# Kernel optimization log

Measured on AMD Instinct MI355X. Metric: run time of the kernel, lower is better.

The kernel has to match this reference:

```python
import jax, jax.numpy as jnp
import numpy as np

N = 8192      # total nodes (32 graphs x 256 nodes)
B = 32        # graphs in batch
E = 65536     # edges per graph (avg degree 16)
DK = 512      # d_k = d_v
H = 32        # mlp / conv channel width
VB = 2048     # body visual dim
VF = 512      # face visual dim
EPS = 1e-5


def setup_inputs() -> dict:
    key = jax.random.key(0)
    ks = jax.random.split(key, 26)
    def n(k, sh, s=1.0):
        return jax.random.normal(k, sh, dtype=jnp.float32) * s
    s2, s512, s32 = 1.0 / np.sqrt(2.0), 1.0 / np.sqrt(512.0), 1.0 / np.sqrt(32.0)
    inp = {}
    inp["x"] = n(ks[0], (N, 2))
    inp["visual_body"] = n(ks[1], (N, VB))
    inp["visual_face"] = n(ks[2], (N, VF))
    # attention projections (no bias)
    inp["Wq"] = n(ks[3], (2, DK), s2)
    inp["Wk"] = n(ks[4], (2, DK), s2)
    inp["Wv"] = n(ks[5], (2, DK), s2)
    # input_mlp: LayerNorm(512) -> PReLU -> Linear(512,32)
    inp["ln_g"] = jnp.ones((DK,), jnp.float32)
    inp["ln_b"] = jnp.zeros((DK,), jnp.float32)
    inp["prelu_a"] = jnp.float32(0.25)
    inp["mlp_W"] = n(ks[6], (DK, H), s512)
    inp["mlp_b"] = jnp.zeros((H,), jnp.float32)
    # node projection Linear(32,1)
    inp["np_W"] = n(ks[7], (H, 1), s32)
    inp["np_b"] = jnp.zeros((1,), jnp.float32)
    # CMCosConv linear weights (32->32) for body / face
    inp["body_W"] = n(ks[8], (H, H), s32)
    inp["body_b"] = jnp.zeros((H,), jnp.float32)
    inp["face_W"] = n(ks[9], (H, H), s32)
    inp["face_b"] = jnp.zeros((H,), jnp.float32)
    # gcn projections Linear(32,1)
    inp["pb_W"] = n(ks[10], (H, 1), s32)
    inp["pb_b"] = jnp.zeros((1,), jnp.float32)
    inp["pf_W"] = n(ks[11], (H, 1), s32)
    inp["pf_b"] = jnp.zeros((1,), jnp.float32)
    # int-valued graph structure
    inp["edge_index_body"] = jax.random.randint(ks[12], (2, E), 0, N)
    inp["edge_index_face"] = jax.random.randint(ks[13], (2, E), 0, N)
    inp["batch_vec"] = jnp.arange(N, dtype=jnp.int64) // (N // B)  # 32 graphs, 256 nodes each
    return inp


def cmcos_conv(x, edge_index, visual, W, b):
    # per-edge cosine(visual_src, visual_dst) * Linear(x_src), scatter-sum to dst
    src, dst = edge_index[0], edge_index[1]
    h = x @ W + b                                          # [N, H]
    vn = visual * jax.lax.rsqrt(jnp.sum(visual * visual, -1, keepdims=True) + 1e-8)
    w = jnp.sum(vn[src] * vn[dst], axis=-1)                # [E] cosine edge weights
    msg = w[:, None] * h[src]                              # [E, H]
    return jax.ops.segment_sum(msg, dst, num_segments=x.shape[0])


def reference(x, visual_body, visual_face, Wq, Wk, Wv, ln_g, ln_b, prelu_a,
              mlp_W, mlp_b, np_W, np_b, body_W, body_b, face_W, face_b,
              pb_W, pb_b, pf_W, pf_b, edge_index_body, edge_index_face, batch_vec):
    sz_b = int(batch_vec[-1]) + 1
    q = (x @ Wq).reshape(sz_b, -1, DK)
    k = (x @ Wk).reshape(sz_b, -1, DK)
    v = (x @ Wv).reshape(sz_b, -1, DK)
    attn = jax.nn.softmax(jnp.einsum('bqd,bkd->bqk', q, k) / np.sqrt(DK), axis=-1)
    out = jnp.einsum('bqk,bkd->bqd', attn, v).reshape(-1, DK)   # [N, 512]
    # input_mlp: LayerNorm -> PReLU -> Linear (dropout is identity in eval)
    mu = jnp.mean(out, -1, keepdims=True)
    var = jnp.mean((out - mu) ** 2, -1, keepdims=True)
    h = (out - mu) * jax.lax.rsqrt(var + EPS) * ln_g + ln_b
    h = jnp.where(h >= 0, h, prelu_a * h)
    h = h @ mlp_W + mlp_b                                       # [N, 32]
    nodes_scores = (h @ np_W + np_b)[:, 0]
    hb = cmcos_conv(h, edge_index_body, visual_body, body_W, body_b)
    hf = cmcos_conv(h, edge_index_face, visual_face, face_W, face_b)
    gcn_scores_body = (hb @ pb_W + pb_b)[:, 0]
    gcn_scores_face = (hf @ pf_W + pf_b)[:, 0]
    return nodes_scores + gcn_scores_body + gcn_scores_face
```

## Files before the change

### kernel.cpp

```cpp
#include <hip/hip_runtime.h>

#define NN 8192
#define NB 32
#define NG 256
#define NE 65536
#define DK 512
#define HC 32
#define DB 2048
#define DF 512

#define BODY_DW (NN*DB/4)
#define FACE_DW (NN*DF/4)
#define B_BODY (BODY_DW/2048)
#define B_FACE (FACE_DW/2048)

typedef float v2f __attribute__((ext_vector_type(2)));

#if __has_builtin(__builtin_amdgcn_cvt_pk_f32_fp8) && __has_builtin(__builtin_amdgcn_cvt_pk_fp8_f32)
#define HW_FP8 1
#else
#define HW_FP8 0
#endif

__device__ __forceinline__ float fp8_dec(unsigned u) {
    unsigned e = (u >> 3) & 15u, m = u & 7u, s = u & 0x80u;
    float v = e ? __uint_as_float(((e + 120u) << 23) | (m << 20))
                : (float)m * 0.001953125f;
    return s ? -v : v;
}
__device__ __forceinline__ unsigned fp8_enc(float x) {
    unsigned sb = (__float_as_uint(x) >> 24) & 0x80u;
    float a = fabsf(x);
    if (a >= 448.f) return sb | 0x7Eu;
    if (a < 0.015625f) {
        int c = (int)rintf(a * 512.f);
        if (c > 7) return sb | 0x08u;
        return sb | (unsigned)c;
    }
    int ex; (void)frexpf(a, &ex);
    float p = ldexpf(a, 1 - ex);
    int m = (int)rintf((p - 1.f) * 8.f);
    int e = ex - 1 + 7;
    if (m == 8) { m = 0; e++; }
    if (e >= 16) return sb | 0x7Eu;
    return sb | (unsigned)(e << 3) | (unsigned)m;
}
__device__ __forceinline__ unsigned pack4_fp8(float x, float y, float z, float w) {
#if HW_FP8
    int u = __builtin_amdgcn_cvt_pk_fp8_f32(x, y, 0, false);
    u = __builtin_amdgcn_cvt_pk_fp8_f32(z, w, u, true);
    return (unsigned)u;
#else
    return fp8_enc(x) | (fp8_enc(y) << 8) | (fp8_enc(z) << 16) | (fp8_enc(w) << 24);
#endif
}
__device__ __forceinline__ float fp8dot4(unsigned a, unsigned b) {
#if HW_FP8
    v2f al = __builtin_amdgcn_cvt_pk_f32_fp8((int)a, false);
    v2f ah = __builtin_amdgcn_cvt_pk_f32_fp8((int)a, true);
    v2f bl = __builtin_amdgcn_cvt_pk_f32_fp8((int)b, false);
    v2f bh = __builtin_amdgcn_cvt_pk_f32_fp8((int)b, true);
    return al.x*bl.x + al.y*bl.y + ah.x*bh.x + ah.y*bh.y;
#else
    float s = 0.f;
    #pragma unroll
    for (int j = 0; j < 4; j++)
        s += fp8_dec((a >> (8*j)) & 255u) * fp8_dec((b >> (8*j)) & 255u);
    return s;
#endif
}
__device__ __forceinline__ float fp8dot16(int4 a, int4 b) {
    return fp8dot4((unsigned)a.x, (unsigned)b.x) + fp8dot4((unsigned)a.y, (unsigned)b.y)
         + fp8dot4((unsigned)a.z, (unsigned)b.z) + fp8dot4((unsigned)a.w, (unsigned)b.w);
}
__device__ __forceinline__ float d4(float4 v) {
    return v.x*v.x + v.y*v.y + v.z*v.z + v.w*v.w;
}

struct Params {
    const float *vb, *vf, *x, *Wq, *Wk, *Wv, *ln_g, *ln_b, *prelu_a;
    const float *mlp_W, *mlp_b, *np_W, *np_b, *body_W, *body_b, *face_W, *face_b;
    const float *pb_W, *pb_b, *pf_W, *pf_b;
    const int *eib, *eif;
    unsigned *vnb, *vnf;
    float *invb, *invf;
    float *a_ws, *sb, *sf, *fused;
    float *out;
};

__global__ __launch_bounds__(256, 4) void k1_kernel(Params p) {
    __shared__ float2 xs[NG];
    __shared__ float pm[4][4];
    __shared__ float sm4[4];
    __shared__ float rss[16];
    const int bid = blockIdx.x, tid = threadIdx.x;
    const int lane = tid & 63, wave = tid >> 6;

    if (bid < B_BODY + B_FACE) {
        const bool body = bid < B_BODY;
        const float4* __restrict__ src = body ? (const float4*)p.vb : (const float4*)p.vf;
        unsigned* __restrict__ dst = body ? p.vnb : p.vnf;
        const int base = (body ? bid : bid - B_BODY) * 2048 + tid;
        if (tid < 16) rss[tid] = 0.f;
        __syncthreads();
        float4 v0 = src[base];
        float4 v1 = src[base + 256];
        float4 v2 = src[base + 512];
        float4 v3 = src[base + 768];
        float4 v4 = src[base + 1024];
        float4 v5 = src[base + 1280];
        float4 v6 = src[base + 1536];
        float4 v7 = src[base + 1792];
        dst[base]        = pack4_fp8(v0.x, v0.y, v0.z, v0.w);
        dst[base + 256]  = pack4_fp8(v1.x, v1.y, v1.z, v1.w);
        dst[base + 512]  = pack4_fp8(v2.x, v2.y, v2.z, v2.w);
        dst[base + 768]  = pack4_fp8(v3.x, v3.y, v3.z, v3.w);
        dst[base + 1024] = pack4_fp8(v4.x, v4.y, v4.z, v4.w);
        dst[base + 1280] = pack4_fp8(v5.x, v5.y, v5.z, v5.w);
        dst[base + 1536] = pack4_fp8(v6.x, v6.y, v6.z, v6.w);
        dst[base + 1792] = pack4_fp8(v7.x, v7.y, v7.z, v7.w);
        if (body) {
            float sq[4];
            sq[0] = d4(v0) + d4(v1);
            sq[1] = d4(v2) + d4(v3);
            sq[2] = d4(v4) + d4(v5);
            sq[3] = d4(v6) + d4(v7);
            #pragma unroll
            for (int r = 0; r < 4; r++) {
                float ss = sq[r];
                #pragma unroll
                for (int off = 32; off > 0; off >>= 1) ss += __shfl_xor(ss, off);
                if (lane == 0) atomicAdd(&rss[r], ss);
            }
            __syncthreads();
            if (tid < 4) p.invb[bid*4 + tid] = rsqrtf(rss[tid] + 1e-8f);
        } else {
            float sq[8] = {d4(v0), d4(v1), d4(v2), d4(v3), d4(v4), d4(v5), d4(v6), d4(v7)};
            #pragma unroll
            for (int j = 0; j < 8; j++) {
                float ss = sq[j];
                #pragma unroll
                for (int off = 32; off > 0; off >>= 1) ss += __shfl_xor(ss, off);
                if (lane == 0) atomicAdd(&rss[(wave >> 1) + 2*j], ss);
            }
            __syncthreads();
            if (tid < 16) p.invf[(bid - B_BODY)*16 + tid] = rsqrtf(rss[tid] + 1e-8f);
        }
        return;
    }
    if (bid < B_BODY + B_FACE + NB) {
        const int gg = bid - (B_BODY + B_FACE);
        xs[tid] = ((const float2*)p.x)[gg*NG + tid];
        const int d = tid * 2;
        float q0a = p.Wq[d],    q0b = p.Wq[d+1];
        float q1a = p.Wq[DK+d], q1b = p.Wq[DK+d+1];
        float k0a = p.Wk[d],    k0b = p.Wk[d+1];
        float k1a = p.Wk[DK+d], k1b = p.Wk[DK+d+1];
        float m00 = q0a*k0a + q0b*k0b;
        float m01 = q0a*k1a + q0b*k1b;
        float m10 = q1a*k0a + q1b*k0b;
        float m11 = q1a*k1a + q1b*k1b;
        #pragma unroll
        for (int off = 32; off > 0; off >>= 1) {
            m00 += __shfl_down(m00,off); m01 += __shfl_down(m01,off);
            m10 += __shfl_down(m10,off); m11 += __shfl_down(m11,off);
        }
        if (lane == 0) { pm[wave][0]=m00; pm[wave][1]=m01; pm[wave][2]=m10; pm[wave][3]=m11; }
        __syncthreads();
        if (tid < 4) sm4[tid] = pm[0][tid] + pm[1][tid] + pm[2][tid] + pm[3][tid];
        __syncthreads();
        const float scale = 0.04419417382415922f;
        const float2 xi = xs[tid];
        const float u0 = (xi.x*sm4[0] + xi.y*sm4[2]) * scale;
        const float u1 = (xi.x*sm4[1] + xi.y*sm4[3]) * scale;
        float m = -1e30f;
        for (int j = 0; j < NG; j++) m = fmaxf(m, u0*xs[j].x + u1*xs[j].y);
        float S = 0.f, a0 = 0.f, a1 = 0.f;
        for (int j = 0; j < NG; j++) {
            float2 xj = xs[j];
            float pr = __expf(u0*xj.x + u1*xj.y - m);
            S += pr; a0 += pr*xj.x; a1 += pr*xj.y;
        }
        const float invS = 1.f / S;
        ((float2*)p.a_ws)[gg*NG + tid] = make_float2(a0*invS, a1*invS);
        return;
    }
    if (tid < HC) {
        float s = 0.f;
        #pragma unroll 8
        for (int c = 0; c < HC; c++) s += p.body_W[tid*HC + c] * p.pb_W[c];
        p.fused[tid] = s;
    } else if (tid < 2*HC) {
        const int cp = tid - HC;
        float s = 0.f;
        #pragma unroll 8
        for (int c = 0; c < HC; c++) s += p.face_W[cp*HC + c] * p.pf_W[c];
        p.fused[HC + cp] = s;
    } else if (tid == 2*HC) {
        float s = 0.f;
        for (int c = 0; c < HC; c++) s += p.body_b[c] * p.pb_W[c];
        p.fused[64] = s;
    } else if (tid == 2*HC + 1) {
        float s = 0.f;
        for (int c = 0; c < HC; c++) s += p.face_b[c] * p.pf_W[c];
        p.fused[65] = s;
    }
}

__global__ __launch_bounds__(256) void k2_kernel(Params p) {
    __shared__ float t[4][DK];
    const int tid = threadIdx.x;
    const int wave = tid >> 6, lane = tid & 63;
    const int node = blockIdx.x * 4 + wave;

    const float a0 = p.a_ws[node*2], a1 = p.a_ws[node*2+1];
    const float4* wv0 = (const float4*)p.Wv;
    const float4* wv1 = (const float4*)(p.Wv + DK);
    const float4* g4 = (const float4*)p.ln_g;
    const float4* b4 = (const float4*)p.ln_b;
    float4 W0[2], W1[2], Gg[2], Bb[2];
    #pragma unroll
    for (int k = 0; k < 2; k++) {
        int c4 = lane*2 + k;
        W0[k] = wv0[c4]; W1[k] = wv1[c4]; Gg[k] = g4[c4]; Bb[k] = b4[c4];
    }
    float s0=0.f, s1=0.f, q00=0.f, q01=0.f, q11=0.f;
    #pragma unroll
    for (int k = 0; k < 2; k++) {
        const float* u = (const float*)&W0[k];
        const float* v = (const float*)&W1[k];
        #pragma unroll
        for (int j = 0; j < 4; j++) {
            s0 += u[j]; s1 += v[j];
            q00 += u[j]*u[j]; q01 += u[j]*v[j]; q11 += v[j]*v[j];
        }
    }
    #pragma unroll
    for (int off = 1; off < 64; off <<= 1) {
        s0 += __shfl_xor(s0,off); s1 += __shfl_xor(s1,off);
        q00 += __shfl_xor(q00,off); q01 += __shfl_xor(q01,off); q11 += __shfl_xor(q11,off);
    }
    const float mean = (a0*s0 + a1*s1) * (1.f/DK);
    const float msq  = (a0*a0*q00 + 2.f*a0*a1*q01 + a1*a1*q11) * (1.f/DK);
    const float inv  = rsqrtf(msq - mean*mean + 1e-5f);
    const float alpha = p.prelu_a[0];
    #pragma unroll
    for (int k = 0; k < 2; k++) {
        int c4 = lane*2 + k;
        const float* u = (const float*)&W0[k];
        const float* v = (const float*)&W1[k];
        const float* gf = (const float*)&Gg[k];
        const float* bf = (const float*)&Bb[k];
        #pragma unroll
        for (int j = 0; j < 4; j++) {
            float od = a0*u[j] + a1*v[j];
            float nd = (od - mean) * inv * gf[j] + bf[j];
            t[wave][c4*4 + j] = (nd >= 0.f) ? nd : alpha*nd;
        }
    }
    __syncthreads();
    const int c = lane & 31, half = lane >> 5;
    const float* tp = t[wave] + half*256;
    const float* mw = p.mlp_W + half*256*HC + c;
    float p0=0.f, p1=0.f, p2=0.f, p3=0.f;
    #pragma unroll 4
    for (int d = 0; d < 256; d += 4) {
        p0 += tp[d]   * mw[d*HC];
        p1 += tp[d+1] * mw[(d+1)*HC];
        p2 += tp[d+2] * mw[(d+2)*HC];
        p3 += tp[d+3] * mw[(d+3)*HC];
    }
    float partl = (p0+p1) + (p2+p3);
    partl += __shfl_down(partl, 32);
    float v0 = 0.f, v1 = 0.f, v2 = 0.f;
    if (lane < 32) {
        float hc = partl + p.mlp_b[c];
        v0 = hc * p.np_W[c];
        v1 = hc * p.fused[c];
        v2 = hc * p.fused[HC + c];
    }
    #pragma unroll
    for (int off = 16; off > 0; off >>= 1) {
        v0 += __shfl_down(v0, off);
        v1 += __shfl_down(v1, off);
        v2 += __shfl_down(v2, off);
    }
    if (lane == 0) {
        p.out[node] = v0 + p.np_b[0] + p.pb_b[0] + p.pf_b[0];
        p.sb[node] = v1 + p.fused[64];
        p.sf[node] = v2 + p.fused[65];
    }
}

__global__ __launch_bounds__(256) void scat_kernel(Params p) {
    const int wave = threadIdx.x >> 6, lane = threadIdx.x & 63;
    if (blockIdx.x < NE/8) {
        const int e = blockIdx.x * 8 + wave * 2;
        const int sA = p.eib[e],     dA = p.eib[NE + e];
        const int sB = p.eib[e + 1], dB = p.eib[NE + e + 1];
        const int4* ap0 = (const int4*)(p.vnb + (size_t)sA * (DB/4));
        const int4* bp0 = (const int4*)(p.vnb + (size_t)dA * (DB/4));
        const int4* ap1 = (const int4*)(p.vnb + (size_t)sB * (DB/4));
        const int4* bp1 = (const int4*)(p.vnb + (size_t)dB * (DB/4));
        int4 a00 = ap0[lane], a01 = ap0[lane + 64];
        int4 b00 = bp0[lane], b01 = bp0[lane + 64];
        int4 a10 = ap1[lane], a11 = ap1[lane + 64];
        int4 b10 = bp1[lane], b11 = bp1[lane + 64];
        float x0 = fp8dot16(a00, b00) + fp8dot16(a01, b01);
        float x1 = fp8dot16(a10, b10) + fp8dot16(a11, b11);
        #pragma unroll
        for (int off = 32; off > 0; off >>= 1) {
            x0 += __shfl_xor(x0, off);
            x1 += __shfl_xor(x1, off);
        }
        if (lane == 0) {
            atomicAdd(&p.out[dA], x0 * p.invb[sA] * p.invb[dA] * p.sb[sA]);
            atomicAdd(&p.out[dB], x1 * p.invb[sB] * p.invb[dB] * p.sb[sB]);
        }
    } else {
        const int e = (blockIdx.x - NE/8) * 16 + wave * 4;
        const int s0 = p.eif[e],     d0 = p.eif[NE + e];
        const int s1 = p.eif[e + 1], d1 = p.eif[NE + e + 1];
        const int s2 = p.eif[e + 2], d2 = p.eif[NE + e + 2];
        const int s3 = p.eif[e + 3], d3 = p.eif[NE + e + 3];
        const int2* ap0 = (const int2*)(p.vnf + (size_t)s0 * (DF/4));
        const int2* bp0 = (const int2*)(p.vnf + (size_t)d0 * (DF/4));
        const int2* ap1 = (const int2*)(p.vnf + (size_t)s1 * (DF/4));
        const int2* bp1 = (const int2*)(p.vnf + (size_t)d1 * (DF/4));
        const int2* ap2 = (const int2*)(p.vnf + (size_t)s2 * (DF/4));
        const int2* bp2 = (const int2*)(p.vnf + (size_t)d2 * (DF/4));
        const int2* ap3 = (const int2*)(p.vnf + (size_t)s3 * (DF/4));
        const int2* bp3 = (const int2*)(p.vnf + (size_t)d3 * (DF/4));
        int2 a0 = ap0[lane], b0 = bp0[lane];
        int2 a1 = ap1[lane], b1 = bp1[lane];
        int2 a2 = ap2[lane], b2 = bp2[lane];
        int2 a3 = ap3[lane], b3 = bp3[lane];
        float x0 = fp8dot4((unsigned)a0.x,(unsigned)b0.x) + fp8dot4((unsigned)a0.y,(unsigned)b0.y);
        float x1 = fp8dot4((unsigned)a1.x,(unsigned)b1.x) + fp8dot4((unsigned)a1.y,(unsigned)b1.y);
        float x2 = fp8dot4((unsigned)a2.x,(unsigned)b2.x) + fp8dot4((unsigned)a2.y,(unsigned)b2.y);
        float x3 = fp8dot4((unsigned)a3.x,(unsigned)b3.x) + fp8dot4((unsigned)a3.y,(unsigned)b3.y);
        #pragma unroll
        for (int off = 32; off > 0; off >>= 1) {
            x0 += __shfl_xor(x0, off);
            x1 += __shfl_xor(x1, off);
            x2 += __shfl_xor(x2, off);
            x3 += __shfl_xor(x3, off);
        }
        if (lane == 0) {
            atomicAdd(&p.out[d0], x0 * p.invf[s0] * p.invf[d0] * p.sf[s0]);
            atomicAdd(&p.out[d1], x1 * p.invf[s1] * p.invf[d1] * p.sf[s1]);
            atomicAdd(&p.out[d2], x2 * p.invf[s2] * p.invf[d2] * p.sf[s2]);
            atomicAdd(&p.out[d3], x3 * p.invf[s3] * p.invf[d3] * p.sf[s3]);
        }
    }
}

extern "C" void kernel_launch(void* const* d_in, const int* in_sizes, int n_in,
                              void* d_out, int out_size, void* d_ws, size_t ws_size,
                              hipStream_t stream) {
    char* ws = (char*)d_ws;
    size_t off = 0;
    auto alloc = [&](size_t bytes) { void* pp = ws + off; off += (bytes + 15) & ~size_t(15); return pp; };

    Params p;
    p.vb      = (const float*)d_in[1];
    p.vf      = (const float*)d_in[2];
    p.x       = (const float*)d_in[0];
    p.Wq      = (const float*)d_in[3];
    p.Wk      = (const float*)d_in[4];
    p.Wv      = (const float*)d_in[5];
    p.ln_g    = (const float*)d_in[6];
    p.ln_b    = (const float*)d_in[7];
    p.prelu_a = (const float*)d_in[8];
    p.mlp_W   = (const float*)d_in[9];
    p.mlp_b   = (const float*)d_in[10];
    p.np_W    = (const float*)d_in[11];
    p.np_b    = (const float*)d_in[12];
    p.body_W  = (const float*)d_in[13];
    p.body_b  = (const float*)d_in[14];
    p.face_W  = (const float*)d_in[15];
    p.face_b  = (const float*)d_in[16];
    p.pb_W    = (const float*)d_in[17];
    p.pb_b    = (const float*)d_in[18];
    p.pf_W    = (const float*)d_in[19];
    p.pf_b    = (const float*)d_in[20];
    p.eib     = (const int*)d_in[21];
    p.eif     = (const int*)d_in[22];
    p.vnb     = (unsigned*)alloc((size_t)BODY_DW*4);
    p.vnf     = (unsigned*)alloc((size_t)FACE_DW*4);
    p.invb    = (float*)alloc((size_t)NN*4);
    p.invf    = (float*)alloc((size_t)NN*4);
    p.a_ws    = (float*)alloc((size_t)NN*2*4);
    p.sb      = (float*)alloc((size_t)NN*4);
    p.sf      = (float*)alloc((size_t)NN*4);
    p.fused   = (float*)alloc((size_t)66*4);
    p.out     = (float*)d_out;

    k1_kernel<<<B_BODY + B_FACE + NB + 1, 256, 0, stream>>>(p);
    k2_kernel<<<NN/4, 256, 0, stream>>>(p);
    scat_kernel<<<NE/8 + NE/16, 256, 0, stream>>>(p);
}
```

Measured before the change: 222.5 us.

## Use fp8 MFMA for edge cosine dots, restructure LN-MLP kernel, precompute Wv stats

The scatter kernel now gives each wave 16 edges and computes their fp8 dot products with 16x16x32 fp8 MFMA instructions. It reads the diagonal of the product, replacing per-lane dot4 conversions and full-wave shuffle reductions. The Wv sum and second-moment statistics move into the k1 tail block, so each k2 wave reads five precomputed scalars instead of reducing them again. k2's 512x32 MLP matvec is rewritten with float4 weight loads and a rotated LDS access pattern. A sched_barrier is added in the fp8 quantize path. The MFMA path computes a full 16x16 block of products but keeps only the diagonal, so 15 of 16 results are discarded, and the gathered operands are strided per edge row.

```diff
diff --git a/kernel.cpp b/kernel.cpp
--- a/kernel.cpp
+++ b/kernel.cpp
@@ -13,13 +13,22 @@
 #define FACE_DW (NN*DF/4)
 #define B_BODY (BODY_DW/2048)
 #define B_FACE (FACE_DW/2048)
+#define WB_BODY (NE/64)
+#define WB_FACE (NE/64)
 
 typedef float v2f __attribute__((ext_vector_type(2)));
+typedef float v4f __attribute__((ext_vector_type(4)));
 
 #if __has_builtin(__builtin_amdgcn_cvt_pk_f32_fp8) && __has_builtin(__builtin_amdgcn_cvt_pk_fp8_f32)
 #define HW_FP8 1
 #else
 #define HW_FP8 0
+#endif
+
+#if __has_builtin(__builtin_amdgcn_mfma_f32_16x16x32_fp8_fp8)
+#define HW_MFMA8 1
+#else
+#define HW_MFMA8 0
 #endif
 
 __device__ __forceinline__ float fp8_dec(unsigned u) {
@@ -68,10 +77,6 @@
         s += fp8_dec((a >> (8*j)) & 255u) * fp8_dec((b >> (8*j)) & 255u);
     return s;
 #endif
-}
-__device__ __forceinline__ float fp8dot16(int4 a, int4 b) {
-    return fp8dot4((unsigned)a.x, (unsigned)b.x) + fp8dot4((unsigned)a.y, (unsigned)b.y)
-         + fp8dot4((unsigned)a.z, (unsigned)b.z) + fp8dot4((unsigned)a.w, (unsigned)b.w);
 }
 __device__ __forceinline__ float d4(float4 v) {
     return v.x*v.x + v.y*v.y + v.z*v.z + v.w*v.w;
@@ -88,11 +93,12 @@
     float *out;
 };
 
-__global__ __launch_bounds__(256, 4) void k1_kernel(Params p) {
+__global__ __launch_bounds__(256) void k1_kernel(Params p) {
     __shared__ float2 xs[NG];
     __shared__ float pm[4][4];
     __shared__ float sm4[4];
     __shared__ float rss[16];
+    __shared__ float wred[4][8];
     const int bid = blockIdx.x, tid = threadIdx.x;
     const int lane = tid & 63, wave = tid >> 6;
 
@@ -111,6 +117,7 @@
         float4 v5 = src[base + 1280];
         float4 v6 = src[base + 1536];
         float4 v7 = src[base + 1792];
+        __builtin_amdgcn_sched_barrier(0);
         dst[base]        = pack4_fp8(v0.x, v0.y, v0.z, v0.w);
         dst[base + 256]  = pack4_fp8(v1.x, v1.y, v1.z, v1.w);
         dst[base + 512]  = pack4_fp8(v2.x, v2.y, v2.z, v2.w);
@@ -185,6 +192,23 @@
         ((float2*)p.a_ws)[gg*NG + tid] = make_float2(a0*invS, a1*invS);
         return;
     }
+    {
+        const int d = tid * 2;
+        float u0 = p.Wv[d], u1 = p.Wv[d+1];
+        float w0 = p.Wv[DK+d], w1 = p.Wv[DK+d+1];
+        float s0 = u0 + u1, s1 = w0 + w1;
+        float q00 = u0*u0 + u1*u1, q01 = u0*w0 + u1*w1, q11 = w0*w0 + w1*w1;
+        #pragma unroll
+        for (int off = 1; off < 64; off <<= 1) {
+            s0 += __shfl_xor(s0,off); s1 += __shfl_xor(s1,off);
+            q00 += __shfl_xor(q00,off); q01 += __shfl_xor(q01,off); q11 += __shfl_xor(q11,off);
+        }
+        if (lane == 0) {
+            wred[wave][0]=s0; wred[wave][1]=s1; wred[wave][2]=q00; wred[wave][3]=q01; wred[wave][4]=q11;
+        }
+        __syncthreads();
+        if (tid < 5) p.fused[66+tid] = wred[0][tid]+wred[1][tid]+wred[2][tid]+wred[3][tid];
+    }
     if (tid < HC) {
         float s = 0.f;
         #pragma unroll 8
@@ -208,82 +232,70 @@
 }
 
 __global__ __launch_bounds__(256) void k2_kernel(Params p) {
-    __shared__ float t[4][DK];
+    __shared__ __align__(16) float t[4][DK];
     const int tid = threadIdx.x;
     const int wave = tid >> 6, lane = tid & 63;
     const int node = blockIdx.x * 4 + wave;
 
     const float a0 = p.a_ws[node*2], a1 = p.a_ws[node*2+1];
-    const float4* wv0 = (const float4*)p.Wv;
-    const float4* wv1 = (const float4*)(p.Wv + DK);
-    const float4* g4 = (const float4*)p.ln_g;
-    const float4* b4 = (const float4*)p.ln_b;
-    float4 W0[2], W1[2], Gg[2], Bb[2];
-    #pragma unroll
-    for (int k = 0; k < 2; k++) {
-        int c4 = lane*2 + k;
-        W0[k] = wv0[c4]; W1[k] = wv1[c4]; Gg[k] = g4[c4]; Bb[k] = b4[c4];
-    }
-    float s0=0.f, s1=0.f, q00=0.f, q01=0.f, q11=0.f;
-    #pragma unroll
-    for (int k = 0; k < 2; k++) {
-        const float* u = (const float*)&W0[k];
-        const float* v = (const float*)&W1[k];
-        #pragma unroll
-        for (int j = 0; j < 4; j++) {
-            s0 += u[j]; s1 += v[j];
-            q00 += u[j]*u[j]; q01 += u[j]*v[j]; q11 += v[j]*v[j];
-        }
-    }
-    #pragma unroll
-    for (int off = 1; off < 64; off <<= 1) {
-        s0 += __shfl_xor(s0,off); s1 += __shfl_xor(s1,off);
-        q00 += __shfl_xor(q00,off); q01 += __shfl_xor(q01,off); q11 += __shfl_xor(q11,off);
-    }
+    const float s0 = p.fused[66], s1 = p.fused[67];
+    const float q00 = p.fused[68], q01 = p.fused[69], q11 = p.fused[70];
     const float mean = (a0*s0 + a1*s1) * (1.f/DK);
     const float msq  = (a0*a0*q00 + 2.f*a0*a1*q01 + a1*a1*q11) * (1.f/DK);
     const float inv  = rsqrtf(msq - mean*mean + 1e-5f);
     const float alpha = p.prelu_a[0];
+
+    const v4f* wv0 = (const v4f*)p.Wv;
+    const v4f* wv1 = (const v4f*)(p.Wv + DK);
+    const v4f* g4 = (const v4f*)p.ln_g;
+    const v4f* b4 = (const v4f*)p.ln_b;
     #pragma unroll
     for (int k = 0; k < 2; k++) {
-        int c4 = lane*2 + k;
-        const float* u = (const float*)&W0[k];
-        const float* v = (const float*)&W1[k];
-        const float* gf = (const float*)&Gg[k];
-        const float* bf = (const float*)&Bb[k];
-        #pragma unroll
-        for (int j = 0; j < 4; j++) {
-            float od = a0*u[j] + a1*v[j];
-            float nd = (od - mean) * inv * gf[j] + bf[j];
-            t[wave][c4*4 + j] = (nd >= 0.f) ? nd : alpha*nd;
-        }
+        const int c4 = lane*2 + k;
+        v4f od = a0*wv0[c4] + a1*wv1[c4];
+        v4f nd = (od - mean) * inv * g4[c4] + b4[c4];
+        v4f pr;
+        pr.x = (nd.x >= 0.f) ? nd.x : alpha*nd.x;
+        pr.y = (nd.y >= 0.f) ? nd.y : alpha*nd.y;
+        pr.z = (nd.z >= 0.f) ? nd.z : alpha*nd.z;
+        pr.w = (nd.w >= 0.f) ? nd.w : alpha*nd.w;
+        *(v4f*)&t[wave][c4*4] = pr;
     }
     __syncthreads();
-    const int c = lane & 31, half = lane >> 5;
-    const float* tp = t[wave] + half*256;
-    const float* mw = p.mlp_W + half*256*HC + c;
-    float p0=0.f, p1=0.f, p2=0.f, p3=0.f;
+
+    const int dg = lane >> 3, c8 = lane & 7;
+    const v4f* W4 = (const v4f*)p.mlp_W;
+    const float* tw = t[wave] + dg*64;
+    v4f h4 = {0.f, 0.f, 0.f, 0.f};
     #pragma unroll 4
-    for (int d = 0; d < 256; d += 4) {
-        p0 += tp[d]   * mw[d*HC];
-        p1 += tp[d+1] * mw[(d+1)*HC];
-        p2 += tp[d+2] * mw[(d+2)*HC];
-        p3 += tp[d+3] * mw[(d+3)*HC];
-    }
-    float partl = (p0+p1) + (p2+p3);
-    partl += __shfl_down(partl, 32);
-    float v0 = 0.f, v1 = 0.f, v2 = 0.f;
-    if (lane < 32) {
-        float hc = partl + p.mlp_b[c];
-        v0 = hc * p.np_W[c];
-        v1 = hc * p.fused[c];
-        v2 = hc * p.fused[HC + c];
+    for (int j = 0; j < 16; j++) {
+        const int dd = ((j + dg*2) & 15) * 4;
+        v4f t4 = *(const v4f*)(tw + dd);
+        const int d = dg*64 + dd;
+        h4 += t4.x * W4[(d+0)*8 + c8]
+            + t4.y * W4[(d+1)*8 + c8]
+            + t4.z * W4[(d+2)*8 + c8]
+            + t4.w * W4[(d+3)*8 + c8];
     }
     #pragma unroll
-    for (int off = 16; off > 0; off >>= 1) {
-        v0 += __shfl_down(v0, off);
-        v1 += __shfl_down(v1, off);
-        v2 += __shfl_down(v2, off);
+    for (int off = 8; off < 64; off <<= 1) {
+        h4.x += __shfl_xor(h4.x, off);
+        h4.y += __shfl_xor(h4.y, off);
+        h4.z += __shfl_xor(h4.z, off);
+        h4.w += __shfl_xor(h4.w, off);
+    }
+    h4 += ((const v4f*)p.mlp_b)[c8];
+    v4f n4 = ((const v4f*)p.np_W)[c8];
+    v4f f4b = ((const v4f*)p.fused)[c8];
+    v4f f4f = ((const v4f*)(p.fused + HC))[c8];
+    float v0 = h4.x*n4.x + h4.y*n4.y + h4.z*n4.z + h4.w*n4.w;
+    float v1 = h4.x*f4b.x + h4.y*f4b.y + h4.z*f4b.z + h4.w*f4b.w;
+    float v2 = h4.x*f4f.x + h4.y*f4f.y + h4.z*f4f.z + h4.w*f4f.w;
+    #pragma unroll
+    for (int off = 1; off < 8; off <<= 1) {
+        v0 += __shfl_xor(v0, off);
+        v1 += __shfl_xor(v1, off);
+        v2 += __shfl_xor(v2, off);
     }
     if (lane == 0) {
         p.out[node] = v0 + p.np_b[0] + p.pb_b[0] + p.pf_b[0];
@@ -294,64 +306,78 @@
 
 __global__ __launch_bounds__(256) void scat_kernel(Params p) {
     const int wave = threadIdx.x >> 6, lane = threadIdx.x & 63;
-    if (blockIdx.x < NE/8) {
-        const int e = blockIdx.x * 8 + wave * 2;
-        const int sA = p.eib[e],     dA = p.eib[NE + e];
-        const int sB = p.eib[e + 1], dB = p.eib[NE + e + 1];
-        const int4* ap0 = (const int4*)(p.vnb + (size_t)sA * (DB/4));
-        const int4* bp0 = (const int4*)(p.vnb + (size_t)dA * (DB/4));
-        const int4* ap1 = (const int4*)(p.vnb + (size_t)sB * (DB/4));
-        const int4* bp1 = (const int4*)(p.vnb + (size_t)dB * (DB/4));
-        int4 a00 = ap0[lane], a01 = ap0[lane + 64];
-        int4 b00 = bp0[lane], b01 = bp0[lane + 64];
-        int4 a10 = ap1[lane], a11 = ap1[lane + 64];
-        int4 b10 = bp1[lane], b11 = bp1[lane + 64];
-        float x0 = fp8dot16(a00, b00) + fp8dot16(a01, b01);
-        float x1 = fp8dot16(a10, b10) + fp8dot16(a11, b11);
+    const int er = lane & 15;
+    const int kb = (lane >> 4) * 8;
+    if (blockIdx.x < WB_BODY) {
+        const int e0 = (blockIdx.x * 4 + wave) * 16;
+        const int s = p.eib[e0 + er];
+        const int d = p.eib[NE + e0 + er];
+        const char* __restrict__ A  = (const char*)p.vnb + (size_t)s * DB + kb;
+        const char* __restrict__ Bq = (const char*)p.vnb + (size_t)d * DB + kb;
+        const float scale = p.invb[s] * p.invb[d] * p.sb[s];
+#if HW_MFMA8
+        v4f acc0 = {0.f,0.f,0.f,0.f}, acc1 = {0.f,0.f,0.f,0.f};
+        #pragma unroll 4
+        for (int k = 0; k < DB; k += 64) {
+            long long a0 = *(const long long*)(A + k);
+            long long b0 = *(const long long*)(Bq + k);
+            long long a1 = *(const long long*)(A + k + 32);
+            long long b1 = *(const long long*)(Bq + k + 32);
+            acc0 = __builtin_amdgcn_mfma_f32_16x16x32_fp8_fp8(a0, b0, acc0, 0, 0, 0);
+            acc1 = __builtin_amdgcn_mfma_f32_16x16x32_fp8_fp8(a1, b1, acc1, 0, 0, 0);
+        }
+        v4f acc = acc0 + acc1;
+        const int row0 = (lane >> 4) * 4;
         #pragma unroll
-        for (int off = 32; off > 0; off >>= 1) {
-            x0 += __shfl_xor(x0, off);
-            x1 += __shfl_xor(x1, off);
-        }
-        if (lane == 0) {
-            atomicAdd(&p.out[dA], x0 * p.invb[sA] * p.invb[dA] * p.sb[sA]);
-            atomicAdd(&p.out[dB], x1 * p.invb[sB] * p.invb[dB] * p.sb[sB]);
-        }
+        for (int r = 0; r < 4; r++)
+            if (row0 + r == er) atomicAdd(&p.out[d], acc[r] * scale);
+#else
+        float part = 0.f;
+        #pragma unroll 4
+        for (int k = 0; k < DB; k += 32) {
+            int2 a = *(const int2*)(A + k);
+            int2 b = *(const int2*)(Bq + k);
+            part += fp8dot4((unsigned)a.x,(unsigned)b.x) + fp8dot4((unsigned)a.y,(unsigned)b.y);
+        }
+        part += __shfl_xor(part, 16);
+        part += __shfl_xor(part, 32);
+        if (lane < 16) atomicAdd(&p.out[d], part * scale);
+#endif
     } else {
-        const int e = (blockIdx.x - NE/8) * 16 + wave * 4;
-        const int s0 = p.eif[e],     d0 = p.eif[NE + e];
-        const int s1 = p.eif[e + 1], d1 = p.eif[NE + e + 1];
-        const int s2 = p.eif[e + 2], d2 = p.eif[NE + e + 2];
-        const int s3 = p.eif[e + 3], d3 = p.eif[NE + e + 3];
-        const int2* ap0 = (const int2*)(p.vnf + (size_t)s0 * (DF/4));
-        const int2* bp0 = (const int2*)(p.vnf + (size_t)d0 * (DF/4));
-        const int2* ap1 = (const int2*)(p.vnf + (size_t)s1 * (DF/4));
-        const int2* bp1 = (const int2*)(p.vnf + (size_t)d1 * (DF/4));
-        const int2* ap2 = (const int2*)(p.vnf + (size_t)s2 * (DF/4));
-        const int2* bp2 = (const int2*)(p.vnf + (size_t)d2 * (DF/4));
-        const int2* ap3 = (const int2*)(p.vnf + (size_t)s3 * (DF/4));
-        const int2* bp3 = (const int2*)(p.vnf + (size_t)d3 * (DF/4));
-        int2 a0 = ap0[lane], b0 = bp0[lane];
-        int2 a1 = ap1[lane], b1 = bp1[lane];
-        int2 a2 = ap2[lane], b2 = bp2[lane];
-        int2 a3 = ap3[lane], b3 = bp3[lane];
-        float x0 = fp8dot4((unsigned)a0.x,(unsigned)b0.x) + fp8dot4((unsigned)a0.y,(unsigned)b0.y);
-        float x1 = fp8dot4((unsigned)a1.x,(unsigned)b1.x) + fp8dot4((unsigned)a1.y,(unsigned)b1.y);
-        float x2 = fp8dot4((unsigned)a2.x,(unsigned)b2.x) + fp8dot4((unsigned)a2.y,(unsigned)b2.y);
-        float x3 = fp8dot4((unsigned)a3.x,(unsigned)b3.x) + fp8dot4((unsigned)a3.y,(unsigned)b3.y);
+        const int e0 = ((blockIdx.x - WB_BODY) * 4 + wave) * 16;
+        const int s = p.eif[e0 + er];
+        const int d = p.eif[NE + e0 + er];
+        const char* __restrict__ A  = (const char*)p.vnf + (size_t)s * DF + kb;
+        const char* __restrict__ Bq = (const char*)p.vnf + (size_t)d * DF + kb;
+        const float scale = p.invf[s] * p.invf[d] * p.sf[s];
+#if HW_MFMA8
+        v4f acc0 = {0.f,0.f,0.f,0.f}, acc1 = {0.f,0.f,0.f,0.f};
+        #pragma unroll 4
+        for (int k = 0; k < DF; k += 64) {
+            long long a0 = *(const long long*)(A + k);
+            long long b0 = *(const long long*)(Bq + k);
+            long long a1 = *(const long long*)(A + k + 32);
+            long long b1 = *(const long long*)(Bq + k + 32);
+            acc0 = __builtin_amdgcn_mfma_f32_16x16x32_fp8_fp8(a0, b0, acc0, 0, 0, 0);
+            acc1 = __builtin_amdgcn_mfma_f32_16x16x32_fp8_fp8(a1, b1, acc1, 0, 0, 0);
+        }
+        v4f acc = acc0 + acc1;
+        const int row0 = (lane >> 4) * 4;
         #pragma unroll
-        for (int off = 32; off > 0; off >>= 1) {
-            x0 += __shfl_xor(x0, off);
-            x1 += __shfl_xor(x1, off);
-            x2 += __shfl_xor(x2, off);
-            x3 += __shfl_xor(x3, off);
-        }
-        if (lane == 0) {
-            atomicAdd(&p.out[d0], x0 * p.invf[s0] * p.invf[d0] * p.sf[s0]);
-            atomicAdd(&p.out[d1], x1 * p.invf[s1] * p.invf[d1] * p.sf[s1]);
-            atomicAdd(&p.out[d2], x2 * p.invf[s2] * p.invf[d2] * p.sf[s2]);
-            atomicAdd(&p.out[d3], x3 * p.invf[s3] * p.invf[d3] * p.sf[s3]);
-        }
+        for (int r = 0; r < 4; r++)
+            if (row0 + r == er) atomicAdd(&p.out[d], acc[r] * scale);
+#else
+        float part = 0.f;
+        #pragma unroll 4
+        for (int k = 0; k < DF; k += 32) {
+            int2 a = *(const int2*)(A + k);
+            int2 b = *(const int2*)(Bq + k);
+            part += fp8dot4((unsigned)a.x,(unsigned)b.x) + fp8dot4((unsigned)a.y,(unsigned)b.y);
+        }
+        part += __shfl_xor(part, 16);
+        part += __shfl_xor(part, 32);
+        if (lane < 16) atomicAdd(&p.out[d], part * scale);
+#endif
     }
 }
 
@@ -393,10 +419,10 @@
     p.a_ws    = (float*)alloc((size_t)NN*2*4);
     p.sb      = (float*)alloc((size_t)NN*4);
     p.sf      = (float*)alloc((size_t)NN*4);
-    p.fused   = (float*)alloc((size_t)66*4);
+    p.fused   = (float*)alloc((size_t)72*4);
     p.out     = (float*)d_out;
 
     k1_kernel<<<B_BODY + B_FACE + NB + 1, 256, 0, stream>>>(p);
     k2_kernel<<<NN/4, 256, 0, stream>>>(p);
-    scat_kernel<<<NE/8 + NE/16, 256, 0, stream>>>(p);
-}
+    scat_kernel<<<WB_BODY + WB_FACE, 256, 0, stream>>>(p);
+}
```

New measurement: 256.9 us. 1.15x slower.
